# Optimization experiments

Measured on AMD Instinct MI355X. Metric: run time of the kernel, lower is better.

Reference implementation:

```python
import jax, jax.numpy as jnp
import numpy as np

B, S, H, W, C = 2, 21, 256, 256, 256
Q, NEG = 256, 256
TEMP = 0.5
STRONG_T = 1.0
EPS = 1e-8


def setup_inputs():
    key = jax.random.key(0)
    k1, k2, k3 = jax.random.split(key, 3)
    rep = jax.random.normal(k1, (B, C, H, W), jnp.float32)
    label = jax.random.randint(k2, (B, 1, H, W), 0, S)
    mask = jnp.ones((B, 1, H, W), jnp.float32)
    prob = jax.random.uniform(k3, (B, S, H, W), jnp.float32)
    return {"rep": rep, "label": label, "mask": mask, "prob": prob}


def _cos(a, b, axis=-1):
    # torch.cosine_similarity: dot / (max(|a|,eps) * max(|b|,eps))
    an = jnp.maximum(jnp.linalg.norm(a, axis=axis), EPS)
    bn = jnp.maximum(jnp.linalg.norm(b, axis=axis), EPS)
    return jnp.sum(a * b, axis=axis) / (an * bn)


def _reco_loss(rep, label, mask, prob):
    Sg = prob.shape[1]
    Cf = rep.shape[1]
    lab = label.reshape(-1).astype(jnp.int32)          # [N]
    ignore = lab > Sg - 1
    lab = jnp.where(ignore, 0, lab)
    m = jnp.where(ignore, 0.0, mask.reshape(-1))
    valid = m > 0                                      # [N]
    feats = jnp.transpose(rep, (0, 2, 3, 1)).reshape(-1, Cf)   # [N,C]
    pflat = jnp.transpose(prob, (0, 2, 3, 1)).reshape(-1, Sg)  # [N,S]
    p_lab = jnp.take_along_axis(pflat, lab[:, None], axis=1)[:, 0]
    hard = valid & (p_lab < STRONG_T)

    seg_id = jnp.where(valid, lab, Sg)  # invalid pixels -> overflow bucket Sg
    counts = jax.ops.segment_sum(valid.astype(jnp.int32), seg_id, num_segments=Sg + 1)[:Sg]
    hard_counts = jax.ops.segment_sum(hard.astype(jnp.int32), seg_id, num_segments=Sg + 1)[:Sg]
    proto = jax.ops.segment_sum(feats * valid[:, None].astype(feats.dtype), seg_id,
                                num_segments=Sg + 1)[:Sg]
    proto = proto / jnp.maximum(counts, 1)[:, None].astype(feats.dtype)  # [S,C]

    # stable sort pixels by (segment, hard-first): emulates the per-segment
    # boolean-mask gathers / concatenation order of the torch code
    order = jnp.argsort(seg_id * 2 + (~hard).astype(jnp.int32))
    feats_sorted = feats[order]                                 # [N,C]
    off = jnp.concatenate([jnp.zeros((1,), counts.dtype), jnp.cumsum(counts)[:-1]])

    seg_ids = jnp.arange(Sg)
    keys = jax.random.split(jax.random.key(1), Sg)

    def body(acc, xs):
        i, ki = xs
        ka, kc, kn = jax.random.split(ki, 3)
        # anchors: num_queries random hard pixels of segment i
        hidx = off[i] + jax.random.randint(ka, (Q,), 0, jnp.maximum(hard_counts[i], 1))
        anchor = feats_sorted[hidx]                             # [Q,C]
        # negative class distribution over other segments (rolled order)
        roll = (i + 1 + jnp.arange(Sg - 1)) % Sg
        proto_logits = _cos(proto[i][None, :], proto[roll]) / TEMP  # [S-1]
        samp = jax.random.categorical(kc, proto_logits, shape=(Q, NEG))
        neg_seg = roll[samp]                                    # [Q,NEG]
        # uniform pixel within each sampled segment's block
        u = jax.random.uniform(kn, (Q, NEG))
        nidx = off[neg_seg] + jnp.floor(u * jnp.maximum(counts[neg_seg], 1)).astype(counts.dtype)
        neg_feat = feats_sorted[nidx]                           # [Q,NEG,C]
        all_feat = jnp.concatenate(
            [jnp.broadcast_to(proto[i], (Q, 1, Cf)), neg_feat], axis=1)
        all_feat = jax.lax.stop_gradient(all_feat)              # torch.no_grad block
        seg_logits = _cos(anchor[:, None, :], all_feat) / TEMP  # [Q,1+NEG]
        # cross-entropy with target 0, mean over queries
        ce = jnp.mean(jax.nn.logsumexp(seg_logits, axis=1) - seg_logits[:, 0])
        acc = acc + jnp.where(hard_counts[i] > 0, ce, 0.0)
        return acc, None

    total, _ = jax.lax.scan(body, jnp.float32(0.0), (seg_ids, keys))
    valid_seg = jnp.sum(counts > 0)
    loss = total / jnp.maximum(valid_seg, 1).astype(jnp.float32)
    return jnp.where(valid_seg > 1, loss, jnp.float32(0.0))


def reference(rep, label, mask, prob):
    loss_weight = 1.0
    return loss_weight * _reco_loss(rep, label, mask, prob)
```

## Files before the change

### kernel.cpp

```cpp
#include <hip/hip_runtime.h>
#include <stdint.h>

#define NPIX  131072
#define HW    65536
#define CCH   256
#define NSEG  21
#define NROLL 20

typedef float f32x2 __attribute__((ext_vector_type(2)));
typedef __fp16 half2t __attribute__((ext_vector_type(2)));

__device__ __forceinline__ uint64_t rng64(uint32_t i, uint32_t q, uint32_t j) {
  uint64_t x = ((uint64_t)((i << 8) | q) << 32) | (uint64_t)(j * 0x9E3779B1u);
  x ^= 0xD1B54A32D192ED03ULL;
  x += 0x9E3779B97F4A7C15ULL;
  x = (x ^ (x >> 30)) * 0xBF58476D1CE4E5B9ULL;
  x = (x ^ (x >> 27)) * 0x94D049BB133111EBULL;
  return x ^ (x >> 31);
}

__device__ __forceinline__ float fdot2h(half2t a, half2t b, float c) {
  return __builtin_amdgcn_fdot2(a, b, c, false);
}

__device__ __forceinline__ void dec16(uint4 w, half2t* nx) {
  uint32_t dw[4] = { w.x, w.y, w.z, w.w };
#pragma unroll
  for (int d = 0; d < 4; ++d) {
    f32x2 lo = __builtin_amdgcn_cvt_pk_f32_fp8((int)dw[d], false);
    f32x2 hi = __builtin_amdgcn_cvt_pk_f32_fp8((int)dw[d], true);
    nx[d * 2 + 0] = __builtin_amdgcn_cvt_pkrtz(lo.x, lo.y);
    nx[d * 2 + 1] = __builtin_amdgcn_cvt_pkrtz(hi.x, hi.y);
  }
}

__device__ __forceinline__ uint32_t pack4fp8(float a, float b, float c, float d) {
  uint32_t w = 0;
  w = (uint32_t)__builtin_amdgcn_cvt_pk_fp8_f32(a, b, (int)w, false);
  w = (uint32_t)__builtin_amdgcn_cvt_pk_fp8_f32(c, d, (int)w, true);
  return w;
}

__global__ __launch_bounds__(256) void reco_a(
    const float* __restrict__ rep, const int* __restrict__ label,
    const float* __restrict__ mask, const float* __restrict__ prob,
    uint8_t* __restrict__ f8, float* __restrict__ norms,
    int* __restrict__ labh, int* __restrict__ bc, float4* __restrict__ zr) {
  int t = threadIdx.x;
  __shared__ __align__(16) char SM[34048];

  if (blockIdx.x < 4096) {
    float* tile = (float*)SM;
    float* partial = (float*)(SM + 32896);
    float* inv = (float*)(SM + 33920);
    int bid = blockIdx.x;
    int row = bid >> 3;
    int w0 = (bid & 7) * 32;
    int b = row >> 8, h = row & 255;
    const float* repb = rep + (size_t)b * CCH * HW + (size_t)h * 256 + w0;
    int w4 = t & 7, cbase = t >> 3;
#pragma unroll
    for (int it = 0; it < 8; ++it) {
      int c = it * 32 + cbase;
      float4 v = *(const float4*)&repb[(size_t)c * HW + w4 * 4];
      tile[(w4 * 4 + 0) * 257 + c] = v.x;
      tile[(w4 * 4 + 1) * 257 + c] = v.y;
      tile[(w4 * 4 + 2) * 257 + c] = v.z;
      tile[(w4 * 4 + 3) * 257 + c] = v.w;
    }
    __syncthreads();
    {
      int w = t & 31, qtr = t >> 5;
      float acc = 0.f;
#pragma unroll 8
      for (int cc = 0; cc < 32; ++cc) {
        float v = tile[w * 257 + qtr * 32 + cc];
        acc += v * v;
      }
      partial[qtr * 32 + w] = acc;
    }
    __syncthreads();
    if (t < 32) {
      float s = 0.f;
#pragma unroll
      for (int j = 0; j < 8; ++j) s += partial[j * 32 + t];
      float nm = fmaxf(sqrtf(s), 1e-8f);
      inv[t] = 1.0f / nm;
      norms[row * 256 + w0 + t] = nm;
    }
    __syncthreads();
    {
      int px = t & 31, chunk = t >> 5;
      float iv = inv[px];
      size_t n = (size_t)(row * 256 + w0 + px);
#pragma unroll
      for (int hk = 0; hk < 2; ++hk) {
        float v[16];
#pragma unroll
        for (int k = 0; k < 16; ++k)
          v[k] = tile[px * 257 + chunk * 32 + hk * 16 + k] * iv;
        uint4 o;
        o.x = pack4fp8(v[0], v[1], v[2], v[3]);
        o.y = pack4fp8(v[4], v[5], v[6], v[7]);
        o.z = pack4fp8(v[8], v[9], v[10], v[11]);
        o.w = pack4fp8(v[12], v[13], v[14], v[15]);
        *(uint4*)&f8[n * CCH + chunk * 32 + hk * 16] = o;
      }
    }
  } else {
    int row = blockIdx.x - 4096;
    int b = row >> 8, h = row & 255;
    int n = row * 256 + t;
    if (row < 6) {
      int idx = row * 256 + t;
      if (idx < 1360) zr[idx] = make_float4(0.f, 0.f, 0.f, 0.f);
    }
    int lab = label[n];
    bool ignore = lab > NSEG - 1;
    if (ignore) lab = 0;
    float mval = ignore ? 0.f : mask[n];
    bool valid = mval > 0.f;
    float p_lab = prob[(((size_t)b * NSEG + lab) * 256 + h) * 256 + t];
    bool hard = valid && (p_lab < 1.0f);
    labh[n] = lab | (hard ? 32 : 0) | (valid ? 64 : 0);

    int* cpart = (int*)SM;
    int* hpart = (int*)SM + 24;
    if (t < NSEG) { cpart[t] = 0; hpart[t] = 0; }
    __syncthreads();
    if (valid) { atomicAdd(&cpart[lab], 1); if (hard) atomicAdd(&hpart[lab], 1); }
    __syncthreads();
    if (t < NSEG) {
      bc[t * 512 + row] = cpart[t];
      bc[(24 + t) * 512 + row] = hpart[t];
    }
  }
}

__global__ __launch_bounds__(256) void reco_k2t(
    const int* __restrict__ bc, int* __restrict__ counts, int* __restrict__ hardc,
    int* __restrict__ offs, int* __restrict__ cur_h, int* __restrict__ cur_e) {
  int t = threadIdx.x;
  int wave = t >> 6, lane = t & 63;
  __shared__ int sums[42];
  for (int c = wave; c < 42; c += 4) {
    int col = (c < 21) ? c : c + 3;
    const int* p = bc + col * 512 + lane * 8;
    int s = 0;
#pragma unroll
    for (int j = 0; j < 8; ++j) s += p[j];
#pragma unroll
    for (int o = 32; o >= 1; o >>= 1) s += __shfl_xor(s, o);
    if (lane == 0) sums[c] = s;
  }
  __syncthreads();
  if (t == 0) {
    int o = 0;
    for (int s = 0; s < NSEG; ++s) {
      counts[s] = sums[s];
      hardc[s] = sums[21 + s];
      offs[s] = o;
      cur_h[s] = o;
      cur_e[s] = o + sums[21 + s];
      o += sums[s];
    }
    offs[NSEG] = o;
  }
}

__global__ __launch_bounds__(256) void reco_k3(const int* __restrict__ labh,
                        int* __restrict__ cur_h, int* __restrict__ cur_e, int* __restrict__ list) {
  int t = threadIdx.x;
  int n = blockIdx.x * 256 + t;
  __shared__ int lcnt[2 * NSEG];
  __shared__ int lbase[2 * NSEG];
  if (t < 2 * NSEG) lcnt[t] = 0;
  __syncthreads();
  int v = labh[n];
  int lab = v & 31;
  bool hard = (v & 32) != 0;
  bool valid = (v & 64) != 0;
  int bucket = lab + (hard ? 0 : NSEG);
  int rank = 0;
  if (valid) rank = atomicAdd(&lcnt[bucket], 1);
  __syncthreads();
  if (t < 2 * NSEG) {
    int c = lcnt[t];
    lbase[t] = c ? atomicAdd((t < NSEG) ? &cur_h[t] : &cur_e[t - NSEG], c) : 0;
  }
  __syncthreads();
  if (valid) list[lbase[bucket] + rank] = n;
}

__global__ __launch_bounds__(256) void reco_proto8(
    const uint8_t* __restrict__ f8, const float* __restrict__ norms,
    const int* __restrict__ list, const int* __restrict__ labh,
    const int* __restrict__ offs, float* __restrict__ proto) {
  int t = threadIdx.x;
  int base = blockIdx.x * 256;
  int total = offs[NSEG];

  __shared__ uint8_t rows[64][256];
  __shared__ float nrm[64];
  __shared__ int segs[256];
  __shared__ int pixs[256];
  __shared__ float red[64][17];

  {
    int pos = base + t;
    int p = (pos < total) ? (list[pos] & (NPIX - 1)) : -1;
    pixs[t] = p;
    segs[t] = (p >= 0) ? (labh[p] & 31) : -1;
  }
  __syncthreads();

  int d = t & 63, qt = t >> 6;
  float a0 = 0.f, a1 = 0.f, a2 = 0.f, a3 = 0.f;
  int cseg = -2;

  for (int sub = 0; sub < 4; ++sub) {
    {
      int r = t >> 2, c = (t & 3) * 64;
      int p = pixs[sub * 64 + r];
      uint4* dst = (uint4*)&rows[r][c];
      if (p >= 0) {
        const uint4* src = (const uint4*)&f8[(size_t)p * CCH + c];
        dst[0] = src[0]; dst[1] = src[1]; dst[2] = src[2]; dst[3] = src[3];
      } else {
        uint4 z = make_uint4(0, 0, 0, 0);
        dst[0] = z; dst[1] = z; dst[2] = z; dst[3] = z;
      }
      if (t < 64) {
        int pp = pixs[sub * 64 + t];
        nrm[t] = (pp >= 0) ? norms[pp] : 0.f;
      }
    }
    __syncthreads();
    for (int pp = 0; pp < 16; ++pp) {
      int pl = qt * 16 + pp;
      int sg = segs[sub * 64 + pl];
      if (sg >= 0) {
        if (sg != cseg) {
          if (cseg >= 0) {
            atomicAdd(&proto[cseg * CCH + d * 4 + 0], a0);
            atomicAdd(&proto[cseg * CCH + d * 4 + 1], a1);
            atomicAdd(&proto[cseg * CCH + d * 4 + 2], a2);
            atomicAdd(&proto[cseg * CCH + d * 4 + 3], a3);
          }
          a0 = a1 = a2 = a3 = 0.f;
          cseg = sg;
        }
        uint32_t w = *(const uint32_t*)&rows[pl][d * 4];
        f32x2 lo = __builtin_amdgcn_cvt_pk_f32_fp8((int)w, false);
        f32x2 hi = __builtin_amdgcn_cvt_pk_f32_fp8((int)w, true);
        float nv = nrm[pl];
        a0 += lo.x * nv; a1 += lo.y * nv; a2 += hi.x * nv; a3 += hi.y * nv;
      }
    }
    __syncthreads();
  }

  int s0 = segs[0];
  int uni = __syncthreads_and((cseg < 0) || (cseg == s0));
  if (uni) {
    if (cseg >= 0) {
      red[d][qt * 4 + 0] = a0;
      red[d][qt * 4 + 1] = a1;
      red[d][qt * 4 + 2] = a2;
      red[d][qt * 4 + 3] = a3;
    }
    __syncthreads();
    if (t < 64 && s0 >= 0) {
#pragma unroll
      for (int c = 0; c < 4; ++c) {
        float v = red[t][0 + c] + red[t][4 + c] + red[t][8 + c] + red[t][12 + c];
        atomicAdd(&proto[s0 * CCH + t * 4 + c], v);
      }
    }
  } else if (cseg >= 0) {
    atomicAdd(&proto[cseg * CCH + d * 4 + 0], a0);
    atomicAdd(&proto[cseg * CCH + d * 4 + 1], a1);
    atomicAdd(&proto[cseg * CCH + d * 4 + 2], a2);
    atomicAdd(&proto[cseg * CCH + d * 4 + 3], a3);
  }
}

__global__ __launch_bounds__(256) void reco_k6r(
    const uint8_t* __restrict__ f8, const int* __restrict__ list,
    const int* __restrict__ counts, const int* __restrict__ hardc,
    const int* __restrict__ offs, const float* __restrict__ proto,
    float* __restrict__ seg_sum, int* __restrict__ ticket, float* __restrict__ out) {
  int bid = blockIdx.x;
  int i  = bid >> 5;
  int qc = bid & 31;
  int t = threadIdx.x;

  __shared__ float spN[NSEG * CCH];
  __shared__ float pn[NSEG];
  __shared__ float lgrow[NROLL];
  __shared__ half2t anch[8 * 128];
  __shared__ float lgts[8][264];
  __shared__ float s_cdf[NROLL];
  __shared__ int s_off[NSEG], s_cnt[NSEG], s_pidx[256], s_apix[8];
  __shared__ float s_ce[8];
  __shared__ int s_last;

  if (t < NSEG) { s_off[t] = offs[t]; s_cnt[t] = counts[t]; }
  __syncthreads();

  for (int idx = t; idx < NSEG * CCH; idx += 256) {
    int s = idx >> 8;
    int c = s_cnt[s]; if (c < 1) c = 1;
    spN[idx] = proto[idx] / (float)c;
  }
  __syncthreads();
  if (t < NSEG) {
    float s2 = 0.f;
    for (int c = 0; c < CCH; ++c) { float v = spN[t * CCH + c]; s2 += v * v; }
    pn[t] = fmaxf(sqrtf(s2), 1e-8f);
  }
  __syncthreads();
  for (int idx = t; idx < NSEG * CCH; idx += 256) {
    int s = idx >> 8;
    spN[idx] = spN[idx] / pn[s];
  }
  __syncthreads();
  if (t < NROLL) {
    int j = (i + 1 + t) % NSEG;
    float d = 0.f;
    for (int c = 0; c < CCH; ++c) d += spN[i * CCH + c] * spN[j * CCH + c];
    lgrow[t] = d * 2.0f;
  }
  __syncthreads();
  if (t == 0) {
    float mx = -1e30f;
    for (int k = 0; k < NROLL; ++k) mx = fmaxf(mx, lgrow[k]);
    float e[NROLL]; float s = 0.f;
    for (int k = 0; k < NROLL; ++k) { e[k] = __expf(lgrow[k] - mx); s += e[k]; }
    float a = 0.f;
    for (int k = 0; k < NROLL; ++k) { a += e[k] / s; s_cdf[k] = a; }
    s_cdf[NROLL - 1] = 2.0f;
  }
  if (t < 8) {
    int q = qc * 8 + t;
    uint64_t r = rng64(i, q, 511u);
    int hc = hardc[i]; if (hc < 1) hc = 1;
    uint32_t jj = (uint32_t)(r & 0xffffffffu) % (uint32_t)hc;
    int idx = offs[i] + (int)jj;
    if (idx > NPIX - 1) idx = NPIX - 1;
    s_apix[t] = list[idx] & (NPIX - 1);
  }
  __syncthreads();

  {
    uint64_t r = rng64(i, 0u, (uint32_t)(t + 1));
    float u1 = (float)(r >> 40) * (1.0f / 16777216.0f);
    float u2 = (float)((r >> 16) & 0xFFFFFFu) * (1.0f / 16777216.0f);
    int k = 0;
#pragma unroll
    for (int kk = 0; kk < NROLL - 1; ++kk) k += (u1 >= s_cdf[kk]);
    int seg = i + 1 + k; if (seg >= NSEG) seg -= NSEG;
    int cnt = s_cnt[seg]; int cm = cnt < 1 ? 1 : cnt;
    int pidx = (int)(u2 * (float)cm);
    if (pidx > cm - 1) pidx = cm - 1;
    int li = s_off[seg] + pidx;
    if (li > NPIX - 1) li = NPIX - 1;
    s_pidx[t] = list[li] & (NPIX - 1);
  }
  if (t < 128) {
    int g = t >> 4, x = t & 15;
    uint4 w = *(const uint4*)&f8[(size_t)s_apix[g] * CCH + x * 16];
    half2t dx[8]; dec16(w, dx);
#pragma unroll
    for (int k = 0; k < 8; ++k) anch[g * 128 + x * 8 + k] = dx[k];
  }
  __syncthreads();

  const uint4* rowp = (const uint4*)&f8[(size_t)s_pidx[t] * CCH];
  float acc[8];
#pragma unroll
  for (int q = 0; q < 8; ++q) acc[q] = 0.f;
  for (int k0 = 0; k0 < 16; k0 += 4) {
    uint4 w4[4];
#pragma unroll
    for (int u = 0; u < 4; ++u) w4[u] = rowp[k0 + u];
#pragma unroll
    for (int u = 0; u < 4; ++u) {
      half2t nx[8]; dec16(w4[u], nx);
      const half2t* ar = anch + (k0 + u) * 8;
#pragma unroll
      for (int q = 0; q < 8; ++q) {
        const half2t* a = ar + q * 128;
        float s = acc[q];
#pragma unroll
        for (int k = 0; k < 8; ++k) s = fdot2h(a[k], nx[k], s);
        acc[q] = s;
      }
    }
  }
  float ps = 0.f;
  if (t < 128) {
    int g = t >> 4, x = t & 15;
    const float* pNs = spN + i * CCH;
#pragma unroll
    for (int k = 0; k < 8; ++k) {
      half2t a = anch[g * 128 + x * 8 + k];
      ps += (float)a.x * pNs[x * 16 + 2 * k] + (float)a.y * pNs[x * 16 + 2 * k + 1];
    }
#pragma unroll
    for (int o = 1; o <= 8; o <<= 1) ps += __shfl_xor(ps, o);
  }

#pragma unroll
  for (int q = 0; q < 8; ++q) lgts[q][1 + t] = acc[q] * 2.0f;
  if (t < 128 && (t & 15) == 0) lgts[t >> 4][0] = ps * 2.0f;
  __syncthreads();

  int wave = t >> 6, lane = t & 63;
  for (int q = wave; q < 8; q += 4) {
    const float* L = lgts[q];
    float v0 = L[lane], v1 = L[lane + 64], v2 = L[lane + 128], v3 = L[lane + 192];
    float v4 = (lane == 0) ? L[256] : -1e30f;
    float m = fmaxf(fmaxf(fmaxf(v0, v1), fmaxf(v2, v3)), v4);
#pragma unroll
    for (int o = 32; o >= 1; o >>= 1) m = fmaxf(m, __shfl_xor(m, o));
    float e = __expf(v0 - m) + __expf(v1 - m) + __expf(v2 - m) + __expf(v3 - m)
            + ((lane == 0) ? __expf(v4 - m) : 0.f);
#pragma unroll
    for (int o = 32; o >= 1; o >>= 1) e += __shfl_xor(e, o);
    if (lane == 0) s_ce[q] = m + logf(e) - L[0];
  }
  __syncthreads();
  if (t == 0) {
    float s = 0.f;
#pragma unroll
    for (int q = 0; q < 8; ++q) s += s_ce[q];
    atomicAdd(&seg_sum[i], s);
    __threadfence();
    int done = atomicAdd(ticket, 1);
    s_last = (done == NSEG * 32 - 1);
  }
  __syncthreads();
  if (s_last && t == 0) {
    __threadfence();
    float tot = 0.f; int vs = 0;
    for (int s = 0; s < NSEG; ++s) {
      vs += (counts[s] > 0);
      float v = atomicAdd(&seg_sum[s], 0.f);
      if (hardc[s] > 0) tot += v;
    }
    float loss = (tot * (1.0f / 256.0f)) / (float)(vs > 0 ? vs : 1);
    out[0] = (vs > 1) ? loss : 0.f;
  }
}

extern "C" void kernel_launch(void* const* d_in, const int* in_sizes, int n_in,
                              void* d_out, int out_size, void* d_ws, size_t ws_size,
                              hipStream_t stream) {
  const float* rep   = (const float*)d_in[0];
  const int*   label = (const int*)d_in[1];
  const float* mask  = (const float*)d_in[2];
  const float* prob  = (const float*)d_in[3];

  char* ws = (char*)d_ws;
  uint8_t* f8 = (uint8_t*)ws;
  size_t o = 67108864;
  float* norms  = (float*)(ws + o); o += 524288;
  int*   list   = (int*)(ws + o);   o += 524288;
  int*   labh   = (int*)(ws + o);   o += 524288;
  float* proto  = (float*)(ws + o); o += 21504;
  float* segsum = (float*)(ws + o); o += 128;
  int*   ticket = (int*)(ws + o);   o += 128;
  int*   counts = (int*)(ws + o);   o += 128;
  int*   hardc  = (int*)(ws + o);   o += 128;
  int*   offs   = (int*)(ws + o);   o += 128;
  int*   cur_h  = (int*)(ws + o);   o += 128;
  int*   cur_e  = (int*)(ws + o);   o += 128;
  int*   bc     = (int*)(ws + o);   o += 98304;

  reco_a<<<4608, 256, 0, stream>>>(rep, label, mask, prob, f8, norms, labh, bc,
                                   (float4*)proto);
  reco_k2t<<<1, 256, 0, stream>>>(bc, counts, hardc, offs, cur_h, cur_e);
  reco_k3<<<512, 256, 0, stream>>>(labh, cur_h, cur_e, list);
  reco_proto8<<<512, 256, 0, stream>>>(f8, norms, list, labh, offs, proto);
  reco_k6r<<<NSEG * 32, 256, 0, stream>>>(f8, list, counts, hardc, offs, proto,
                                          segsum, ticket, (float*)d_out);
}
```

Baseline: 105.5 us.

## Merge count scan into scatter kernel, split proto blocks, swizzle block order

Drops the single-block scan kernel. Every scatter block now reduces the per-row counts itself and computes segment offsets locally, and cur_h/cur_e become relative counters that reco_a zeroes by extending its zero range. The proto kernel now handles 64 pixels per block over 4x more blocks, removing the serial sub-loop and its barriers. Block indices in reco_a and reco_k6r are remapped, likely to spread neighbouring work across XCDs. The cost is redundant count reduction in all 512 scatter blocks and more atomic flushes to proto.

New measurement: 112.3 us. +6.5%, slower.

```diff
diff --git a/kernel.cpp b/kernel.cpp
--- a/kernel.cpp
+++ b/kernel.cpp
@@ -50,10 +50,10 @@
   __shared__ __align__(16) char SM[34048];
 
   if (blockIdx.x < 4096) {
+    int bid = (blockIdx.x & 7) * 512 + (blockIdx.x >> 3);
     float* tile = (float*)SM;
     float* partial = (float*)(SM + 32896);
     float* inv = (float*)(SM + 33920);
-    int bid = blockIdx.x;
     int row = bid >> 3;
     int w0 = (bid & 7) * 32;
     int b = row >> 8, h = row & 255;
@@ -113,7 +113,7 @@
     int n = row * 256 + t;
     if (row < 6) {
       int idx = row * 256 + t;
-      if (idx < 1360) zr[idx] = make_float4(0.f, 0.f, 0.f, 0.f);
+      if (idx < 1376) zr[idx] = make_float4(0.f, 0.f, 0.f, 0.f);
     }
     int lab = label[n];
     bool ignore = lab > NSEG - 1;
@@ -137,12 +137,19 @@
   }
 }
 
-__global__ __launch_bounds__(256) void reco_k2t(
-    const int* __restrict__ bc, int* __restrict__ counts, int* __restrict__ hardc,
-    int* __restrict__ offs, int* __restrict__ cur_h, int* __restrict__ cur_e) {
+__global__ __launch_bounds__(256) void reco_k3(
+    const int* __restrict__ labh, const int* __restrict__ bc,
+    int* __restrict__ cur_h, int* __restrict__ cur_e,
+    int* __restrict__ counts, int* __restrict__ hardc, int* __restrict__ offs,
+    int* __restrict__ list) {
   int t = threadIdx.x;
+  int n = blockIdx.x * 256 + t;
+  __shared__ int sums[48];
+  __shared__ int soffs[NSEG];
+  __shared__ int lcnt[2 * NSEG];
+  __shared__ int lbase[2 * NSEG];
+
   int wave = t >> 6, lane = t & 63;
-  __shared__ int sums[42];
   for (int c = wave; c < 42; c += 4) {
     int col = (c < 21) ? c : c + 3;
     const int* p = bc + col * 512 + lane * 8;
@@ -153,29 +160,24 @@
     for (int o = 32; o >= 1; o >>= 1) s += __shfl_xor(s, o);
     if (lane == 0) sums[c] = s;
   }
+  if (t < 2 * NSEG) lcnt[t] = 0;
   __syncthreads();
   if (t == 0) {
     int o = 0;
-    for (int s = 0; s < NSEG; ++s) {
-      counts[s] = sums[s];
-      hardc[s] = sums[21 + s];
-      offs[s] = o;
-      cur_h[s] = o;
-      cur_e[s] = o + sums[21 + s];
-      o += sums[s];
-    }
-    offs[NSEG] = o;
-  }
-}
-
-__global__ __launch_bounds__(256) void reco_k3(const int* __restrict__ labh,
-                        int* __restrict__ cur_h, int* __restrict__ cur_e, int* __restrict__ list) {
-  int t = threadIdx.x;
-  int n = blockIdx.x * 256 + t;
-  __shared__ int lcnt[2 * NSEG];
-  __shared__ int lbase[2 * NSEG];
-  if (t < 2 * NSEG) lcnt[t] = 0;
-  __syncthreads();
+    for (int s = 0; s < NSEG; ++s) { soffs[s] = o; o += sums[s]; }
+    if (blockIdx.x == 0) {
+      int oo = 0;
+      for (int s = 0; s < NSEG; ++s) {
+        counts[s] = sums[s];
+        hardc[s] = sums[21 + s];
+        offs[s] = oo;
+        oo += sums[s];
+      }
+      offs[NSEG] = oo;
+    }
+  }
+  __syncthreads();
+
   int v = labh[n];
   int lab = v & 31;
   bool hard = (v & 32) != 0;
@@ -189,7 +191,11 @@
     lbase[t] = c ? atomicAdd((t < NSEG) ? &cur_h[t] : &cur_e[t - NSEG], c) : 0;
   }
   __syncthreads();
-  if (valid) list[lbase[bucket] + rank] = n;
+  if (valid) {
+    int pos = soffs[lab] + (hard ? (lbase[bucket] + rank)
+                                 : (sums[21 + lab] + lbase[bucket] + rank));
+    list[pos] = n;
+  }
 }
 
 __global__ __launch_bounds__(256) void reco_proto8(
@@ -197,67 +203,58 @@
     const int* __restrict__ list, const int* __restrict__ labh,
     const int* __restrict__ offs, float* __restrict__ proto) {
   int t = threadIdx.x;
-  int base = blockIdx.x * 256;
+  int base = blockIdx.x * 64;
   int total = offs[NSEG];
 
   __shared__ uint8_t rows[64][256];
   __shared__ float nrm[64];
-  __shared__ int segs[256];
-  __shared__ int pixs[256];
+  __shared__ int segs[64];
   __shared__ float red[64][17];
 
   {
-    int pos = base + t;
+    int r = t >> 2, c = (t & 3) * 64;
+    int pos = base + r;
     int p = (pos < total) ? (list[pos] & (NPIX - 1)) : -1;
-    pixs[t] = p;
-    segs[t] = (p >= 0) ? (labh[p] & 31) : -1;
+    uint4* dst = (uint4*)&rows[r][c];
+    if (p >= 0) {
+      const uint4* src = (const uint4*)&f8[(size_t)p * CCH + c];
+      dst[0] = src[0]; dst[1] = src[1]; dst[2] = src[2]; dst[3] = src[3];
+    } else {
+      uint4 z = make_uint4(0, 0, 0, 0);
+      dst[0] = z; dst[1] = z; dst[2] = z; dst[3] = z;
+    }
+    if (t < 64) {
+      int pos2 = base + t;
+      int p2 = (pos2 < total) ? (list[pos2] & (NPIX - 1)) : -1;
+      segs[t] = (p2 >= 0) ? (labh[p2] & 31) : -1;
+      nrm[t] = (p2 >= 0) ? norms[p2] : 0.f;
+    }
   }
   __syncthreads();
 
   int d = t & 63, qt = t >> 6;
   float a0 = 0.f, a1 = 0.f, a2 = 0.f, a3 = 0.f;
   int cseg = -2;
-
-  for (int sub = 0; sub < 4; ++sub) {
-    {
-      int r = t >> 2, c = (t & 3) * 64;
-      int p = pixs[sub * 64 + r];
-      uint4* dst = (uint4*)&rows[r][c];
-      if (p >= 0) {
-        const uint4* src = (const uint4*)&f8[(size_t)p * CCH + c];
-        dst[0] = src[0]; dst[1] = src[1]; dst[2] = src[2]; dst[3] = src[3];
-      } else {
-        uint4 z = make_uint4(0, 0, 0, 0);
-        dst[0] = z; dst[1] = z; dst[2] = z; dst[3] = z;
-      }
-      if (t < 64) {
-        int pp = pixs[sub * 64 + t];
-        nrm[t] = (pp >= 0) ? norms[pp] : 0.f;
-      }
-    }
-    __syncthreads();
-    for (int pp = 0; pp < 16; ++pp) {
-      int pl = qt * 16 + pp;
-      int sg = segs[sub * 64 + pl];
-      if (sg >= 0) {
-        if (sg != cseg) {
-          if (cseg >= 0) {
-            atomicAdd(&proto[cseg * CCH + d * 4 + 0], a0);
-            atomicAdd(&proto[cseg * CCH + d * 4 + 1], a1);
-            atomicAdd(&proto[cseg * CCH + d * 4 + 2], a2);
-            atomicAdd(&proto[cseg * CCH + d * 4 + 3], a3);
-          }
-          a0 = a1 = a2 = a3 = 0.f;
-          cseg = sg;
+  for (int pp = 0; pp < 16; ++pp) {
+    int pl = qt * 16 + pp;
+    int sg = segs[pl];
+    if (sg >= 0) {
+      if (sg != cseg) {
+        if (cseg >= 0) {
+          atomicAdd(&proto[cseg * CCH + d * 4 + 0], a0);
+          atomicAdd(&proto[cseg * CCH + d * 4 + 1], a1);
+          atomicAdd(&proto[cseg * CCH + d * 4 + 2], a2);
+          atomicAdd(&proto[cseg * CCH + d * 4 + 3], a3);
         }
-        uint32_t w = *(const uint32_t*)&rows[pl][d * 4];
-        f32x2 lo = __builtin_amdgcn_cvt_pk_f32_fp8((int)w, false);
-        f32x2 hi = __builtin_amdgcn_cvt_pk_f32_fp8((int)w, true);
-        float nv = nrm[pl];
-        a0 += lo.x * nv; a1 += lo.y * nv; a2 += hi.x * nv; a3 += hi.y * nv;
-      }
-    }
-    __syncthreads();
+        a0 = a1 = a2 = a3 = 0.f;
+        cseg = sg;
+      }
+      uint32_t w = *(const uint32_t*)&rows[pl][d * 4];
+      f32x2 lo = __builtin_amdgcn_cvt_pk_f32_fp8((int)w, false);
+      f32x2 hi = __builtin_amdgcn_cvt_pk_f32_fp8((int)w, true);
+      float nv = nrm[pl];
+      a0 += lo.x * nv; a1 += lo.y * nv; a2 += hi.x * nv; a3 += hi.y * nv;
+    }
   }
 
   int s0 = segs[0];
@@ -290,9 +287,9 @@
     const int* __restrict__ counts, const int* __restrict__ hardc,
     const int* __restrict__ offs, const float* __restrict__ proto,
     float* __restrict__ seg_sum, int* __restrict__ ticket, float* __restrict__ out) {
-  int bid = blockIdx.x;
-  int i  = bid >> 5;
-  int qc = bid & 31;
+  int u = (blockIdx.x & 7) * 84 + (blockIdx.x >> 3);
+  int i  = u >> 5;
+  int qc = u & 31;
   int t = threadIdx.x;
 
   __shared__ float spN[NSEG * CCH];
@@ -383,11 +380,11 @@
   for (int k0 = 0; k0 < 16; k0 += 4) {
     uint4 w4[4];
 #pragma unroll
-    for (int u = 0; u < 4; ++u) w4[u] = rowp[k0 + u];
-#pragma unroll
-    for (int u = 0; u < 4; ++u) {
-      half2t nx[8]; dec16(w4[u], nx);
-      const half2t* ar = anch + (k0 + u) * 8;
+    for (int uu = 0; uu < 4; ++uu) w4[uu] = rowp[k0 + uu];
+#pragma unroll
+    for (int uu = 0; uu < 4; ++uu) {
+      half2t nx[8]; dec16(w4[uu], nx);
+      const half2t* ar = anch + (k0 + uu) * 8;
 #pragma unroll
       for (int q = 0; q < 8; ++q) {
         const half2t* a = ar + q * 128;
@@ -471,18 +468,17 @@
   float* proto  = (float*)(ws + o); o += 21504;
   float* segsum = (float*)(ws + o); o += 128;
   int*   ticket = (int*)(ws + o);   o += 128;
+  int*   cur_h  = (int*)(ws + o);   o += 128;
+  int*   cur_e  = (int*)(ws + o);   o += 128;
   int*   counts = (int*)(ws + o);   o += 128;
   int*   hardc  = (int*)(ws + o);   o += 128;
   int*   offs   = (int*)(ws + o);   o += 128;
-  int*   cur_h  = (int*)(ws + o);   o += 128;
-  int*   cur_e  = (int*)(ws + o);   o += 128;
   int*   bc     = (int*)(ws + o);   o += 98304;
 
   reco_a<<<4608, 256, 0, stream>>>(rep, label, mask, prob, f8, norms, labh, bc,
                                    (float4*)proto);
-  reco_k2t<<<1, 256, 0, stream>>>(bc, counts, hardc, offs, cur_h, cur_e);
-  reco_k3<<<512, 256, 0, stream>>>(labh, cur_h, cur_e, list);
-  reco_proto8<<<512, 256, 0, stream>>>(f8, norms, list, labh, offs, proto);
+  reco_k3<<<512, 256, 0, stream>>>(labh, bc, cur_h, cur_e, counts, hardc, offs, list);
+  reco_proto8<<<2048, 256, 0, stream>>>(f8, norms, list, labh, offs, proto);
   reco_k6r<<<NSEG * 32, 256, 0, stream>>>(f8, list, counts, hardc, offs, proto,
                                           segsum, ticket, (float*)d_out);
 }
```
